# Optimization experiments

Hardware: AMD Instinct MI355X
Metric: run time of the kernel (lower is better)

## Reference

```python
import math
import jax, jax.numpy as jnp
import numpy as np


def _shift_matrix(kmax):
    # Faithful translation of EPG_shift_matrices (flat-index fill, reshape, transpose)
    N = (kmax + 1) * 3
    S = np.zeros((N * N,), np.float32)
    kidx = list(range(3, N, 3)); sidx = [x - 3 for x in kidx]
    S[[a + b for a, b in zip(kidx, [N * x for x in sidx])]] = 1
    kidx = list(range(4, N, 3)); kidx.pop(); sidx = [x + 3 for x in kidx]
    S[[a + b for a, b in zip(kidx, [N * x for x in sidx])]] = 1
    kidx = list(range(2, N, 3))
    S[[a + b for a, b in zip(kidx, [N * x for x in kidx])]] = 1
    S = S.reshape(N, N).T.copy()
    S[0:2, 4] = 1
    return jnp.asarray(S)


def _rf_rot_ex(alpha):
    c2, s2 = math.cos(alpha / 2.0) ** 2, math.sin(alpha / 2.0) ** 2
    c, s = math.cos(alpha), math.sin(alpha)
    return jnp.asarray(np.array([[c2, -s2, s], [-s2, c2, s], [-0.5 * s, -0.5 * s, c]], np.float32))


def _rf_rot_refoc(alpha):
    c2, s2 = math.cos(alpha / 2.0) ** 2, math.sin(alpha / 2.0) ** 2
    c, s = math.cos(alpha), math.sin(alpha)
    return jnp.asarray(np.array([[c2, s2, s], [s2, c2, -s], [-0.5 * s, 0.5 * s, c]], np.float32))


def _epg_tse(theta, ESP, T1, T2, z0, inversion, TI):
    # theta: python list of flip angles; T1,T2,z0: (im_dim, 1) arrays
    np2 = len(theta)
    kmax = 2 * (np2 - 1)
    kpp = np.array([2 * x + 1 for x in list(range(1, math.ceil(np2 / 2) + 1))
                    + list(range(math.floor(np2 / 2), 0, -1))])
    kpp[kpp > kmax] = kmax
    if kpp.max() < kmax:
        kmax = int(kpp.max())
    N = 3 * (kmax + 1)
    im_dim = T1.shape[0]
    S = _shift_matrix(kmax)                                   # (N, N)
    E1 = jnp.exp(-0.5 * ESP / T1)                             # (im, 1)
    E2 = jnp.exp(-0.5 * ESP / T2)                             # (im, 1)
    Ed = jnp.concatenate([E2, E2, E1], axis=1)[:, :, None] * jnp.eye(3, dtype=T1.dtype)  # (im,3,3)
    b = jnp.zeros((im_dim, N, 1), T1.dtype).at[:, 2, :].set(1 - E1)
    Ik = jnp.eye(kmax + 1, dtype=T1.dtype)
    Efull = jnp.einsum('ij,nkl->nikjl', Ik, Ed).reshape(im_dim, N, N)  # kron(I, Ed)
    ES = Efull @ S                                            # (im, N, N)
    F = jnp.zeros((im_dim, N, np2 - 1), T1.dtype)
    FF = jnp.zeros((im_dim, N, 1), T1.dtype).at[:, 2, :].set(z0)
    if inversion:
        d = jnp.exp(-TI / T1)
        FF = FF.at[:, 2, :].set(d * (-FF[:, 2, :]) + 1 - d)
    A = _rf_rot_ex(abs(theta[0]))
    FF = FF.at[:, :3].set(A @ FF[:, :3])
    FF = FF.at[:, :6].set(ES[:, :6, :6] @ FF[:, :6] + b[:, :6])
    A = _rf_rot_refoc(abs(theta[1]))
    T = jnp.kron(Ik, A)                                       # block-diag refocusing op (N, N)
    for jj in range(1, np2):                                  # static loop over echo pulses
        K = 3 * int(kpp[jj])
        ff = T[:K, :K] @ FF[:, :K]                            # (im, K, 1)
        FF = FF.at[:, :K].set(ff)
        fcol = ES[:, :K, :K] @ ff + b[:, :K]                  # (im, K, 1)
        F = F.at[:, :K, jj - 1].set(fcol[:, :, 0])
        if jj == np2 - 1:
            break
        FF = FF.at[:, :K].set(ES[:, :K, :K] @ fcol + b[:, :K])
    return F[:, 0, :], F[:, 2::3, :]                          # s (im, np2-1), Zn (im, kmax+1, np2-1)


def setup_inputs():
    key = jax.random.key(0)
    fake_param = jax.random.uniform(key, (1, 3, 16384, 1), jnp.float32)
    return {"fake_param": fake_param, "nrefocus": 16, "ESP": 10, "TE": 80,
            "TR": 3000, "inversion": 0, "TI": 0}


def reference(fake_param, nrefocus, ESP, TE, TR, inversion, TI):
    PD = fake_param[0, 0]                  # (im, 1)
    T1 = fake_param[0, 1] * 5000 + 0.01
    T2 = fake_param[0, 2] * 1500 + 0.01
    if nrefocus == 1:
        a0 = [70 * math.pi / 180, math.pi]
        Ntr = 5
    else:
        a0 = [math.pi / 2] + [120 * math.pi / 180] * nrefocus
        Ntr = 2
    Xi = jnp.exp(-(TR - ESP * (nrefocus + 0.5)) / T1)
    z0 = PD
    for _ in range(Ntr):
        s, Zn = _epg_tse(a0, ESP, T1, T2, z0, inversion, TI)
        z0 = Xi * Zn[:, 0, -1][:, None] + 1 - Xi
    return jnp.abs(s[:, math.ceil(TE / ESP) - 1]) * PD[:, 0]
```

## Files before the change

### kernel.cpp

```cpp
#include <hip/hip_runtime.h>
#include <math.h>

#define PI_F 3.14159265358979323846f

template <int CTRL>
__device__ __forceinline__ float qperm(float x) {
    return __int_as_float(
        __builtin_amdgcn_mov_dpp(__float_as_int(x), CTRL, 0xF, 0xF, true));
}
#define QP_UP   0x90
#define QP_DOWN 0xF9

template <int CUT>
__device__ __forceinline__ void es4(float (&Fp)[5], float (&Fm)[5], float (&Z)[5],
                                    int g, float E1, float E2, float b2l) {
    float fpin = qperm<QP_UP>(Fp[4]);
    float fmin = qperm<QP_DOWN>(Fm[0]);
    float src0 = (g == 0) ? Fm[1] : fpin;
    Fp[4] = E2 * Fp[3];
    Fp[3] = E2 * Fp[2];
    Fp[2] = E2 * Fp[1];
    Fp[1] = E2 * Fp[0];
    Fp[0] = E2 * src0;
    Fm[0] = E2 * Fm[1];
    Fm[1] = E2 * Fm[2];
    Fm[2] = E2 * Fm[3];
    Fm[3] = E2 * Fm[4];
    Fm[4] = E2 * fmin;
    if (g == CUT / 5) Fm[CUT % 5] = 0.f;
    Z[0] = fmaf(Z[0], E1, b2l);
    Z[1] *= E1; Z[2] *= E1; Z[3] *= E1; Z[4] *= E1;
}

__device__ __forceinline__ void rot4(float (&Fp)[5], float (&Fm)[5], float (&Z)[5],
                                     float c2, float s2, float s, float hs, float c) {
#pragma unroll
    for (int j = 0; j < 5; ++j) {
        float x = Fp[j], y = Fm[j], z = Z[j];
        Fp[j] = c2 * x + s2 * y + s * z;
        Fm[j] = s2 * x + c2 * y - s * z;
        Z[j]  = hs * (y - x) + c * z;
    }
}

__device__ __forceinline__ int kpp_of(int j, int np2) {
    int cei = (np2 + 1) / 2, flo = np2 / 2, km0 = 2 * (np2 - 1);
    int v = (j < cei) ? (2 * (j + 1) + 1) : (2 * (flo - (j - cei)) + 1);
    return v > km0 ? km0 : v;
}

template <int NT_MAX>
__device__ __forceinline__ void apply_ES(float (&FF)[3 * NT_MAX], int nt,
                                         float E1, float E2, float b2) {
    float t4 = FF[4];
#pragma unroll
    for (int k = NT_MAX - 1; k >= 1; --k)
        if (k < nt) FF[3 * k] = E2 * FF[3 * k - 3];
    FF[0] = E2 * t4;
    FF[1] = E2 * t4;
#pragma unroll
    for (int k = 1; k <= NT_MAX - 2; ++k)
        if (k < nt - 1) FF[3 * k + 1] = E2 * FF[3 * k + 4];
#pragma unroll
    for (int k = 1; k < NT_MAX; ++k)
        if (k == nt - 1) FF[3 * k + 1] = 0.f;
#pragma unroll
    for (int k = 0; k < NT_MAX; ++k)
        if (k < nt) FF[3 * k + 2] *= E1;
    FF[2] += b2;
}

template <int NT_MAX>
__device__ __forceinline__ void rotate_all(float (&FF)[3 * NT_MAX], int nt,
                                           float c2, float s2, float s, float c) {
#pragma unroll
    for (int k = 0; k < NT_MAX; ++k) {
        if (k < nt) {
            float x = FF[3 * k], y = FF[3 * k + 1], z = FF[3 * k + 2];
            FF[3 * k]     = c2 * x + s2 * y + s * z;
            FF[3 * k + 1] = s2 * x + c2 * y - s * z;
            FF[3 * k + 2] = -0.5f * s * x + 0.5f * s * y + c * z;
        }
    }
}

template <int NT_MAX>
__device__ __forceinline__ void epg_tse_scalar(int np2, float z0, int inversion, float TIf,
                                               float T1, float E1, float E2,
                                               float sex, float cex,
                                               float rc2, float rs2, float rs, float rc,
                                               int te_idx, float& s_out, float& z_out) {
    float FF[3 * NT_MAX];
#pragma unroll
    for (int i = 0; i < 3 * NT_MAX; ++i) FF[i] = 0.f;
    float z = z0;
    if (inversion) { float d = expf(-TIf / T1); z = d * (-z) + 1.f - d; }
    FF[0] = sex * z; FF[1] = sex * z; FF[2] = cex * z;
    float b2 = 1.f - E1;
    apply_ES<NT_MAX>(FF, 2, E1, E2, b2);
    s_out = 0.f; z_out = 0.f;
    for (int jj = 1; jj < np2; ++jj) {
        int nt = kpp_of(jj, np2);
        rotate_all<NT_MAX>(FF, nt, rc2, rs2, rs, rc);
        apply_ES<NT_MAX>(FF, nt, E1, E2, b2);
        if (jj - 1 == te_idx) s_out = FF[0];
        if (jj == np2 - 1) { z_out = FF[2]; }
        else apply_ES<NT_MAX>(FF, nt, E1, E2, b2);
    }
}

__global__ __launch_bounds__(256) void epg_kernel(
    const float* __restrict__ fp, const int* __restrict__ nrefp,
    const int* __restrict__ espp, const int* __restrict__ tep,
    const int* __restrict__ trp, const int* __restrict__ invp,
    const int* __restrict__ tip, float* __restrict__ out, int im) {
    int tid = blockIdx.x * blockDim.x + threadIdx.x;
    int p = tid >> 2;
    int g = tid & 3;
    if (p >= im) return;

    int nref = nrefp[0], ESP = espp[0], TE = tep[0], TR = trp[0];
    int inv = invp[0], TI = tip[0];

    float PD = fp[p];
    float T1 = fp[im + p] * 5000.f + 0.01f;
    float T2 = fp[2 * im + p] * 1500.f + 0.01f;

    int np2, Ntr;
    float aex, aref;
    if (nref == 1) { np2 = 2; aex = 70.f * PI_F / 180.f; aref = PI_F; Ntr = 5; }
    else           { np2 = nref + 1; aex = 0.5f * PI_F; aref = 120.f * PI_F / 180.f; Ntr = 2; }

    float Xi = expf(-((float)TR - (float)ESP * ((float)nref + 0.5f)) / T1);
    float E1 = expf(-0.5f * (float)ESP / T1);
    float E2 = expf(-0.5f * (float)ESP / T2);
    int te_idx = (TE + ESP - 1) / ESP - 1;

    float sex = sinf(aex), cex = cosf(aex);
    float ch = cosf(0.5f * aref), sh = sinf(0.5f * aref);
    float rc2 = ch * ch, rs2 = sh * sh, rs = sinf(aref), rc = cosf(aref);
    float rhs = 0.5f * rs;
    float b2 = 1.f - E1;
    float b2l = (g == 0) ? b2 : 0.f;

    float z0 = PD, s_te = 0.f;

    if (np2 == 17) {
        for (int tr = 0; tr < Ntr; ++tr) {
            float Fp[5], Fm[5], Z[5];
#pragma unroll
            for (int j = 0; j < 5; ++j) { Fp[j] = 0.f; Fm[j] = 0.f; Z[j] = 0.f; }
            float ez = z0;
            if (inv) { float d = expf(-(float)TI / T1); ez = d * (-ez) + 1.f - d; }
            if (g == 0) { Fp[0] = sex * ez; Fm[0] = sex * ez; Z[0] = cex * ez; }
            es4<1>(Fp, Fm, Z, g, E1, E2, b2l);

            float s_val = 0.f, zl = 0.f;
#define ECHO(JJ, NT)                                             \
            rot4(Fp, Fm, Z, rc2, rs2, rs, rhs, rc);              \
            es4<(NT) - 1>(Fp, Fm, Z, g, E1, E2, b2l);            \
            if ((JJ) - 1 == te_idx) s_val = Fp[0];               \
            if ((JJ) == 16) zl = Z[0];                           \
            else es4<(NT) - 1>(Fp, Fm, Z, g, E1, E2, b2l);

            ECHO(1, 5)  ECHO(2, 7)  ECHO(3, 9)  ECHO(4, 11)
            ECHO(5, 13) ECHO(6, 15) ECHO(7, 17) ECHO(8, 19)
            ECHO(9, 17) ECHO(10, 15) ECHO(11, 13) ECHO(12, 11)
            ECHO(13, 9) ECHO(14, 7)  ECHO(15, 5)  ECHO(16, 3)
#undef ECHO
            z0 = Xi * zl + 1.f - Xi;
            s_te = s_val;
        }
    } else if (np2 <= 17) {
        for (int tr = 0; tr < Ntr; ++tr) {
            float s, zl;
            epg_tse_scalar<20>(np2, z0, inv, (float)TI, T1, E1, E2, sex, cex,
                               rc2, rs2, rs, rc, te_idx, s, zl);
            z0 = Xi * zl + 1.f - Xi;
            s_te = s;
        }
    } else {
        for (int tr = 0; tr < Ntr; ++tr) {
            float s, zl;
            epg_tse_scalar<40>(np2, z0, inv, (float)TI, T1, E1, E2, sex, cex,
                               rc2, rs2, rs, rc, te_idx, s, zl);
            z0 = Xi * zl + 1.f - Xi;
            s_te = s;
        }
    }

    if (g == 0) out[p] = fabsf(s_te) * PD;
}

extern "C" void kernel_launch(void* const* d_in, const int* in_sizes, int n_in,
                              void* d_out, int out_size, void* d_ws, size_t ws_size,
                              hipStream_t stream) {
    const float* fp  = (const float*)d_in[0];
    const int* nrefp = (const int*)d_in[1];
    const int* espp  = (const int*)d_in[2];
    const int* tep   = (const int*)d_in[3];
    const int* trp   = (const int*)d_in[4];
    const int* invp  = (const int*)d_in[5];
    const int* tip   = (const int*)d_in[6];
    float* out       = (float*)d_out;

    int im = out_size;
    int threads = im * 4;
    int block = 256;
    int grid = (threads + block - 1) / block;
    hipLaunchKernelGGL(epg_kernel, dim3(grid), dim3(block), 0, stream,
                       fp, nrefp, espp, tep, trp, invp, tip, out, im);
}
```

Measured before the change: 11.74 us.

## Fuse relaxation-shift pairs into rotation with folded constants for nref=16

Adds a specialized path for nrefocus==16 in which the two relaxation/shift steps around each refocusing pulse are merged algebraically. The E1/E2 decay factors are folded into the rotation coefficients, the double shift becomes a two-position DPP lane exchange, and the refocusing angle trigonometry is replaced by hard-coded constants. It also uses fast __expf. The intent is to cut per-echo ALU work and cross-lane permutes. In exchange it divides by E1 and E2 to recover intermediate values, which risks precision loss or bad values when the decays are very small.

```diff
diff --git a/kernel.cpp b/kernel.cpp
--- a/kernel.cpp
+++ b/kernel.cpp
@@ -11,36 +11,39 @@
 #define QP_UP   0x90
 #define QP_DOWN 0xF9
 
-template <int CUT>
-__device__ __forceinline__ void es4(float (&Fp)[5], float (&Fm)[5], float (&Z)[5],
-                                    int g, float E1, float E2, float b2l) {
-    float fpin = qperm<QP_UP>(Fp[4]);
-    float fmin = qperm<QP_DOWN>(Fm[0]);
-    float src0 = (g == 0) ? Fm[1] : fpin;
-    Fp[4] = E2 * Fp[3];
-    Fp[3] = E2 * Fp[2];
-    Fp[2] = E2 * Fp[1];
-    Fp[1] = E2 * Fp[0];
-    Fp[0] = E2 * src0;
-    Fm[0] = E2 * Fm[1];
-    Fm[1] = E2 * Fm[2];
-    Fm[2] = E2 * Fm[3];
-    Fm[3] = E2 * Fm[4];
-    Fm[4] = E2 * fmin;
-    if (g == CUT / 5) Fm[CUT % 5] = 0.f;
-    Z[0] = fmaf(Z[0], E1, b2l);
-    Z[1] *= E1; Z[2] *= E1; Z[3] *= E1; Z[4] *= E1;
-}
-
-__device__ __forceinline__ void rot4(float (&Fp)[5], float (&Fm)[5], float (&Z)[5],
-                                     float c2, float s2, float s, float hs, float c) {
+template <int NT>
+__device__ __forceinline__ void fecho(float (&wFp)[5], float (&wFm)[5], float (&wZ)[5],
+                                      int g, bool g0, int jj, int te_idx, bool last,
+                                      float q2c2, float q2s2, float q2s,
+                                      float e2hs, float e2c,
+                                      float invE2, float invE1, float b2, float b2tl,
+                                      float& s_val, float& zl) {
+    float rx[5], ry[5], rz[5];
 #pragma unroll
     for (int j = 0; j < 5; ++j) {
-        float x = Fp[j], y = Fm[j], z = Z[j];
-        Fp[j] = c2 * x + s2 * y + s * z;
-        Fm[j] = s2 * x + c2 * y - s * z;
-        Z[j]  = hs * (y - x) + c * z;
-    }
+        float x = wFp[j], y = wFm[j], z = wZ[j];
+        rx[j] = q2c2 * x + q2s2 * y + q2s * z;
+        ry[j] = q2s2 * x + q2c2 * y - q2s * z;
+        rz[j] = e2hs * (y - x) + e2c * z;
+    }
+    if (jj - 1 == te_idx) s_val = ry[1] * invE2;
+    if (last)             zl    = rz[0] * invE1 + b2;
+
+    float upA = qperm<QP_UP>(rx[3]);
+    float upB = qperm<QP_UP>(rx[4]);
+    float dnA = qperm<QP_DOWN>(ry[0]);
+    float dnB = qperm<QP_DOWN>(ry[1]);
+
+    wFp[0] = g0 ? ry[2] : upA;
+    wFp[1] = g0 ? ry[1] : upB;
+    wFp[2] = rx[0]; wFp[3] = rx[1]; wFp[4] = rx[2];
+    wFm[0] = ry[2]; wFm[1] = ry[3]; wFm[2] = ry[4];
+    wFm[3] = dnA;   wFm[4] = dnB;
+    constexpr int C1 = NT - 1, C0 = NT - 2;
+    if (g == C1 / 5) wFm[C1 % 5] = 0.f;
+    if (g == C0 / 5) wFm[C0 % 5] = 0.f;
+    wZ[0] = rz[0] + b2tl;
+    wZ[1] = rz[1]; wZ[2] = rz[2]; wZ[3] = rz[3]; wZ[4] = rz[4];
 }
 
 __device__ __forceinline__ int kpp_of(int j, int np2) {
@@ -118,6 +121,7 @@
     int p = tid >> 2;
     int g = tid & 3;
     if (p >= im) return;
+    bool g0 = (g == 0);
 
     int nref = nrefp[0], ESP = espp[0], TE = tep[0], TR = trp[0];
     int inv = invp[0], TI = tip[0];
@@ -125,6 +129,45 @@
     float PD = fp[p];
     float T1 = fp[im + p] * 5000.f + 0.01f;
     float T2 = fp[2 * im + p] * 1500.f + 0.01f;
+
+    int te_idx = (TE + ESP - 1) / ESP - 1;
+
+    if (nref == 16) {
+        float Xi = __expf(-((float)TR - (float)ESP * 16.5f) / T1);
+        float E1 = __expf(-0.5f * (float)ESP / T1);
+        float E2 = __expf(-0.5f * (float)ESP / T2);
+        float b2 = 1.f - E1;
+        const float c2 = 0.25f, s2 = 0.75f, s = 0.8660254037844387f, c = -0.5f;
+        float e22 = E2 * E2, e12 = E1 * E1;
+        float q2c2 = e22 * c2, q2s2 = e22 * s2, q2s = e22 * s;
+        float e2hs = e12 * 0.5f * s, e2c = e12 * c;
+        float invE2 = (E2 >= 1e-30f) ? 1.f / E2 : 0.f;
+        float invE1 = (E1 >= 1e-30f) ? 1.f / E1 : 0.f;
+        float b2tl = g0 ? b2 * (1.f + E1) : 0.f;
+
+        float z0 = PD, s_te = 0.f;
+        for (int tr = 0; tr < 2; ++tr) {
+            float ez = z0;
+            if (inv) { float d = __expf(-(float)TI / T1); ez = d * (-ez) + 1.f - d; }
+            float wFp[5] = {0.f, 0.f, 0.f, 0.f, 0.f};
+            float wFm[5] = {0.f, 0.f, 0.f, 0.f, 0.f};
+            float wZ[5]  = {0.f, 0.f, 0.f, 0.f, 0.f};
+            if (g0) { wFp[1] = E2 * ez; wZ[0] = b2; }
+
+            float s_val = 0.f, zl = 0.f;
+#define FE(JJ, NT) fecho<NT>(wFp, wFm, wZ, g, g0, JJ, te_idx, (JJ) == 16, \
+                             q2c2, q2s2, q2s, e2hs, e2c, invE2, invE1, b2, b2tl, s_val, zl);
+            FE(1, 5)   FE(2, 7)   FE(3, 9)   FE(4, 11)
+            FE(5, 13)  FE(6, 15)  FE(7, 17)  FE(8, 19)
+            FE(9, 17)  FE(10, 15) FE(11, 13) FE(12, 11)
+            FE(13, 9)  FE(14, 7)  FE(15, 5)  FE(16, 3)
+#undef FE
+            z0 = Xi * zl + 1.f - Xi;
+            s_te = s_val;
+        }
+        if (g0) out[p] = fabsf(s_te) * PD;
+        return;
+    }
 
     int np2, Ntr;
     float aex, aref;
@@ -134,44 +177,13 @@
     float Xi = expf(-((float)TR - (float)ESP * ((float)nref + 0.5f)) / T1);
     float E1 = expf(-0.5f * (float)ESP / T1);
     float E2 = expf(-0.5f * (float)ESP / T2);
-    int te_idx = (TE + ESP - 1) / ESP - 1;
 
     float sex = sinf(aex), cex = cosf(aex);
     float ch = cosf(0.5f * aref), sh = sinf(0.5f * aref);
     float rc2 = ch * ch, rs2 = sh * sh, rs = sinf(aref), rc = cosf(aref);
-    float rhs = 0.5f * rs;
-    float b2 = 1.f - E1;
-    float b2l = (g == 0) ? b2 : 0.f;
 
     float z0 = PD, s_te = 0.f;
-
-    if (np2 == 17) {
-        for (int tr = 0; tr < Ntr; ++tr) {
-            float Fp[5], Fm[5], Z[5];
-#pragma unroll
-            for (int j = 0; j < 5; ++j) { Fp[j] = 0.f; Fm[j] = 0.f; Z[j] = 0.f; }
-            float ez = z0;
-            if (inv) { float d = expf(-(float)TI / T1); ez = d * (-ez) + 1.f - d; }
-            if (g == 0) { Fp[0] = sex * ez; Fm[0] = sex * ez; Z[0] = cex * ez; }
-            es4<1>(Fp, Fm, Z, g, E1, E2, b2l);
-
-            float s_val = 0.f, zl = 0.f;
-#define ECHO(JJ, NT)                                             \
-            rot4(Fp, Fm, Z, rc2, rs2, rs, rhs, rc);              \
-            es4<(NT) - 1>(Fp, Fm, Z, g, E1, E2, b2l);            \
-            if ((JJ) - 1 == te_idx) s_val = Fp[0];               \
-            if ((JJ) == 16) zl = Z[0];                           \
-            else es4<(NT) - 1>(Fp, Fm, Z, g, E1, E2, b2l);
-
-            ECHO(1, 5)  ECHO(2, 7)  ECHO(3, 9)  ECHO(4, 11)
-            ECHO(5, 13) ECHO(6, 15) ECHO(7, 17) ECHO(8, 19)
-            ECHO(9, 17) ECHO(10, 15) ECHO(11, 13) ECHO(12, 11)
-            ECHO(13, 9) ECHO(14, 7)  ECHO(15, 5)  ECHO(16, 3)
-#undef ECHO
-            z0 = Xi * zl + 1.f - Xi;
-            s_te = s_val;
-        }
-    } else if (np2 <= 17) {
+    if (np2 <= 17) {
         for (int tr = 0; tr < Ntr; ++tr) {
             float s, zl;
             epg_tse_scalar<20>(np2, z0, inv, (float)TI, T1, E1, E2, sex, cex,
@@ -188,8 +200,7 @@
             s_te = s;
         }
     }
-
-    if (g == 0) out[p] = fabsf(s_te) * PD;
+    if (g0) out[p] = fabsf(s_te) * PD;
 }
 
 extern "C" void kernel_launch(void* const* d_in, const int* in_sizes, int n_in,
```

Measured after the change: 11.44 us. -2.5%, faster.
